# Kernel tuning notes

Hardware: AMD Instinct MI355X
Metric: run time of the kernel (lower is better)

Reference implementation:

```python
import jax, jax.numpy as jnp
import numpy as np

N_LAYERS = 2   # number of S6 blocks
D = 512        # input_dim / d_model
N = 16         # hid_dim (SSM state size)
O = 512        # output_dim
B = 4          # batch
L = 2048       # seq_len
LN_EPS = 1e-5


def setup_inputs() -> dict:
    key = jax.random.key(0)
    ks = jax.random.split(key, 10)
    s = D ** -0.5
    inp = {
        "x": jax.random.normal(ks[0], (B, L, D), jnp.float32),
        # per-layer S6 block params (stacked over layer axis)
        "A_log": jax.random.normal(ks[1], (N_LAYERS, D, N), jnp.float32) * 0.5,
        "W_B": jax.random.normal(ks[2], (N_LAYERS, D, N), jnp.float32) * s,
        "b_B": jnp.zeros((N_LAYERS, N), jnp.float32),
        "W_C": jax.random.normal(ks[3], (N_LAYERS, D, N), jnp.float32) * s,
        "b_C": jnp.zeros((N_LAYERS, N), jnp.float32),
        "W_dt": jax.random.normal(ks[4], (N_LAYERS, D, D), jnp.float32) * s,
        "b_dt": jnp.zeros((N_LAYERS, D), jnp.float32),
        "D_skip": jnp.ones((N_LAYERS, D), jnp.float32),
        # mixing linear + layer norm per layer
        "W_mix": jax.random.normal(ks[5], (N_LAYERS, D, D), jnp.float32) * s,
        "b_mix": jnp.zeros((N_LAYERS, D), jnp.float32),
        "ln_g": jnp.ones((N_LAYERS, D), jnp.float32),
        "ln_b": jnp.zeros((N_LAYERS, D), jnp.float32),
        # final decoder
        "W_dec": jax.random.normal(ks[6], (D, O), jnp.float32) * s,
        "b_dec": jnp.zeros((O,), jnp.float32),
    }
    return inp


def _combine(e1, e2):
    # first-order linear recurrence combine: h <- a*h + u
    a1, u1 = e1
    a2, u2 = e2
    return a1 * a2, a2 * u1 + u2


def reference(x, A_log, W_B, b_B, W_C, b_C, W_dt, b_dt, D_skip,
              W_mix, b_mix, ln_g, ln_b, W_dec, b_dec):
    h_in = x  # [B, L, D]
    for i in range(N_LAYERS):
        # ---- S6 block: input-dependent B, C, dt; diagonal A ----
        A = -jnp.exp(A_log[i])                               # [D, N], negative real
        Bm = h_in @ W_B[i] + b_B[i]                          # [B, L, N]
        Cm = h_in @ W_C[i] + b_C[i]                          # [B, L, N]
        dt = jax.nn.softplus(h_in @ W_dt[i] + b_dt[i])       # [B, L, D]
        # discretize: a_t = exp(dt*A), u_t = dt * B_t * x_t
        a = jnp.exp(dt[..., None] * A)                       # [B, L, D, N]
        u = (dt * h_in)[..., None] * Bm[:, :, None, :]       # [B, L, D, N]
        # parallel scan over sequence axis (Heinsen / Blelloch style)
        _, h = jax.lax.associative_scan(_combine, (a, u), axis=1)
        y = jnp.einsum('bln,bldn->bld', Cm, h) + D_skip[i] * h_in  # [B, L, D]
        # ---- activation (torch.nn.GELU default = exact erf) ----
        y = jax.nn.gelu(y, approximate=False)
        # ---- mixing linear ----
        y = y @ W_mix[i] + b_mix[i]
        # ---- layer norm ----
        mu = jnp.mean(y, axis=-1, keepdims=True)
        var = jnp.var(y, axis=-1, keepdims=True)
        y = (y - mu) / jnp.sqrt(var + LN_EPS) * ln_g[i] + ln_b[i]
        # ---- residual ----
        h_in = h_in + y
    return h_in @ W_dec + b_dec  # [B, L, O]
```

## Files before the change

### kernel.cpp

```cpp
#include <hip/hip_runtime.h>
#include <math.h>

typedef unsigned short u16;
typedef unsigned int u32;
typedef __attribute__((ext_vector_type(8))) short short8;
typedef __attribute__((ext_vector_type(4))) float f32x4;

#define BL 8192
#define DD 512
#define NN 16
#define NCHUNK 64
#define SCH 32
#define ZLD 640

__device__ __forceinline__ u16 f2bf(float f) {
  union { float f; u32 u; } v; v.f = f;
  u32 u = v.u;
  return (u16)((u + 0x7FFFu + ((u >> 16) & 1u)) >> 16);
}

__device__ __forceinline__ void split2(float v, u16* __restrict__ h,
                                       u16* __restrict__ l) {
  union { float f; u32 u; } a; a.f = v;
  u32 hr = (a.u + 0x7FFFu + ((a.u >> 16) & 1u)) & 0xFFFF0000u;
  union { u32 u; float f; } hv; hv.u = hr;
  float r = v - hv.f;
  *h = (u16)(hr >> 16);
  *l = f2bf(r);
}

__device__ __forceinline__ float comb2(u16 h, u16 l) {
  union { u32 u; float f; } a, b;
  a.u = (u32)h << 16; b.u = (u32)l << 16;
  return a.f + b.f;
}

__device__ __forceinline__ float softplus_f(float z) {
  float w = __builtin_amdgcn_exp2f(-1.4426950408889634f * fabsf(z));
  return fmaxf(z, 0.0f) + 0.69314718055994531f * __builtin_amdgcn_logf(1.0f + w);
}

__device__ __forceinline__ float gelu_erf(float y) {
  float ax = fabsf(y) * 0.70710678118654752f;
  float t  = __builtin_amdgcn_rcpf(1.0f + 0.3275911f * ax);
  float e  = __builtin_amdgcn_exp2f(-1.4426950408889634f * ax * ax);
  float p  = ((((1.061405429f * t - 1.453152027f) * t + 1.421413741f) * t
               - 0.284496736f) * t + 0.254829592f) * t;
  float er = copysignf(1.0f - p * e, y);
  return 0.5f * y * (1.0f + er);
}

#define PREP_TOT (4194304 + 655360 + 524288 + 262144 + 1280 + 16384)
__global__ __launch_bounds__(256) void prep_kernel(
    const float* __restrict__ x, const float* __restrict__ A_log,
    const float* __restrict__ W_B, const float* __restrict__ b_B,
    const float* __restrict__ W_C, const float* __restrict__ b_C,
    const float* __restrict__ W_dt, const float* __restrict__ b_dt,
    const float* __restrict__ W_mix, const float* __restrict__ W_dec,
    u16* __restrict__ xh, u16* __restrict__ xl,
    u16* __restrict__ Wch, u16* __restrict__ Wcl,
    u16* __restrict__ Wmh, u16* __restrict__ Wml,
    u16* __restrict__ Wdh, u16* __restrict__ Wdl,
    float* __restrict__ bcat, float* __restrict__ A2)
{
  int i = blockIdx.x * 256 + threadIdx.x;
  if (i >= PREP_TOT) return;
  if (i < 4194304) { split2(x[i], &xh[i], &xl[i]); return; }
  i -= 4194304;
  if (i < 655360) {
    int l = i / 327680, r = i % 327680, n = r >> 9, k = r & 511;
    float v = 0.0f;
    if (n < 16)       v = W_B[l * 8192 + k * 16 + n];
    else if (n < 32)  v = W_C[l * 8192 + k * 16 + (n - 16)];
    else if (n < 544) v = W_dt[l * 262144 + k * 512 + (n - 32)];
    split2(v, &Wch[i], &Wcl[i]);
    return;
  }
  i -= 655360;
  if (i < 524288) {
    int l = i / 262144, r = i % 262144, n = r >> 9, k = r & 511;
    split2(W_mix[l * 262144 + k * 512 + n], &Wmh[i], &Wml[i]);
    return;
  }
  i -= 524288;
  if (i < 262144) {
    int n = i >> 9, k = i & 511;
    split2(W_dec[k * 512 + n], &Wdh[i], &Wdl[i]);
    return;
  }
  i -= 262144;
  if (i < 1280) {
    int l = i / 640, n = i % 640;
    float v = 0.0f;
    if (n < 16)       v = b_B[l * 16 + n];
    else if (n < 32)  v = b_C[l * 16 + (n - 16)];
    else if (n < 544) v = b_dt[l * 512 + (n - 32)];
    bcat[i] = v;
    return;
  }
  i -= 1280;
  A2[i] = -expf(A_log[i]) * 1.4426950408889634f;
}

template <int MODE>
__global__ __launch_bounds__(256) void gemm_bt(
    const u16* __restrict__ Ah, const u16* __restrict__ Al,
    const u16* __restrict__ Bh, const u16* __restrict__ Bl,
    const float* __restrict__ bias, float* __restrict__ Cmat, int ldc,
    int NX)
{
  const int K = 512;
  int bid = blockIdx.x;
  int xcd = bid & 7;
  int rest = bid >> 3;
  int mloc = rest & 7;
  int nb = rest >> 3;
  int m0 = (xcd * 8 + mloc) * 128;
  int n0 = nb * 64;
  __shared__ __align__(16) char smem[36864];
  u16* Ash = (u16*)smem;
  u16* Asl = Ash + 128 * 32;
  u16* Bsh = Asl + 128 * 32;
  u16* Bsl = Bsh + 64 * 32;
  int tid = threadIdx.x;
  int wave = tid >> 6, lane = tid & 63;
  int wm = (wave >> 1) * 64;
  int wn = (wave & 1) * 32;
  int lrow = lane & 15;
  int lk = (lane >> 4) * 8;
  f32x4 acc[4][2] = {};

  int q0 = tid, q1 = tid + 256;
  size_t offA0 = (size_t)(m0 + (q0 >> 2)) * K + (q0 & 3) * 8;
  size_t offA1 = (size_t)(m0 + (q1 >> 2)) * K + (q1 & 3) * 8;
  size_t offB  = (size_t)(n0 + (q0 >> 2)) * K + (q0 & 3) * 8;
  unsigned l0 = (unsigned)(wave * 64) * 8;
  unsigned l1 = (unsigned)(wave * 64 + 256) * 8;

  for (int k0 = 0; k0 < K; k0 += 32) {
    __builtin_amdgcn_global_load_lds(
        (const __attribute__((address_space(1))) void*)(Ah + offA0 + k0),
        (__attribute__((address_space(3))) void*)(&Ash[l0]), 16, 0, 0);
    __builtin_amdgcn_global_load_lds(
        (const __attribute__((address_space(1))) void*)(Ah + offA1 + k0),
        (__attribute__((address_space(3))) void*)(&Ash[l1]), 16, 0, 0);
    __builtin_amdgcn_global_load_lds(
        (const __attribute__((address_space(1))) void*)(Al + offA0 + k0),
        (__attribute__((address_space(3))) void*)(&Asl[l0]), 16, 0, 0);
    __builtin_amdgcn_global_load_lds(
        (const __attribute__((address_space(1))) void*)(Al + offA1 + k0),
        (__attribute__((address_space(3))) void*)(&Asl[l1]), 16, 0, 0);
    __builtin_amdgcn_global_load_lds(
        (const __attribute__((address_space(1))) void*)(Bh + offB + k0),
        (__attribute__((address_space(3))) void*)(&Bsh[l0]), 16, 0, 0);
    __builtin_amdgcn_global_load_lds(
        (const __attribute__((address_space(1))) void*)(Bl + offB + k0),
        (__attribute__((address_space(3))) void*)(&Bsl[l0]), 16, 0, 0);
    __syncthreads();

    short8 afh[4], afl[4], bfh[2], bfl[2];
#pragma unroll
    for (int i = 0; i < 4; ++i) {
      afh[i] = *(const short8*)&Ash[(wm + i * 16 + lrow) * 32 + lk];
      afl[i] = *(const short8*)&Asl[(wm + i * 16 + lrow) * 32 + lk];
    }
#pragma unroll
    for (int t = 0; t < 2; ++t) {
      bfh[t] = *(const short8*)&Bsh[(wn + t * 16 + lrow) * 32 + lk];
      bfl[t] = *(const short8*)&Bsl[(wn + t * 16 + lrow) * 32 + lk];
    }
#pragma unroll
    for (int i = 0; i < 4; ++i)
#pragma unroll
      for (int t = 0; t < 2; ++t) {
        acc[i][t] = __builtin_amdgcn_mfma_f32_16x16x32_bf16(afh[i], bfh[t], acc[i][t], 0, 0, 0);
        acc[i][t] = __builtin_amdgcn_mfma_f32_16x16x32_bf16(afl[i], bfh[t], acc[i][t], 0, 0, 0);
        acc[i][t] = __builtin_amdgcn_mfma_f32_16x16x32_bf16(afh[i], bfl[t], acc[i][t], 0, 0, 0);
      }
    __syncthreads();
  }

  float* ct = (float*)smem + wave * (64 * 36);
  int quad = lane >> 4;
#pragma unroll
  for (int t = 0; t < 2; ++t) {
    int coll = wn + t * 16 + lrow;
    float bv = bias[n0 + coll];
    bool sp = (MODE == 1) && (n0 + coll >= 32);
#pragma unroll
    for (int i = 0; i < 4; ++i) {
#pragma unroll
      for (int r = 0; r < 4; ++r) {
        float v = acc[i][t][r] + bv;
        if (sp) v = softplus_f(v);
        ct[(i * 16 + quad * 4 + r) * 36 + (t * 16 + lrow)] = v;
      }
    }
  }
  __syncthreads();
  int r8 = lane >> 3, c8 = lane & 7;
  int colv = n0 + wn + c8 * 4;
  bool do_store = !(MODE == 1 && colv >= 544);
#pragma unroll
  for (int pass = 0; pass < 8; ++pass) {
    int rowl = pass * 8 + r8;
    float4 v = *(const float4*)&ct[rowl * 36 + c8 * 4];
    if (do_store)
      *(float4*)&Cmat[(size_t)(m0 + wm + rowl) * ldc + colv] = v;
  }
}

template <int PACKED>
__global__ __launch_bounds__(256) void scan_p1(
    const float* __restrict__ Z, const float* __restrict__ Xf,
    const u16* __restrict__ Xh, const u16* __restrict__ Xl,
    const float* __restrict__ A2,
    float* __restrict__ Ach, float* __restrict__ Uch)
{
  int bid = blockIdx.x;
  int dg = bid & 1, c = (bid >> 1) & (NCHUNK - 1), b = bid >> 7;
  int d = dg * 256 + threadIdx.x;
  int row0 = b * 2048 + c * SCH;
  __shared__ float Bsh[SCH * 16];
  for (int i = threadIdx.x; i < SCH * 16; i += 256)
    Bsh[i] = Z[(size_t)(row0 + (i >> 4)) * ZLD + (i & 15)];
  __syncthreads();
  float a2[16];
  const float4* a2v = (const float4*)(A2 + d * 16);
#pragma unroll
  for (int q = 0; q < 4; ++q) {
    float4 f = a2v[q];
    a2[q * 4 + 0] = f.x; a2[q * 4 + 1] = f.y; a2[q * 4 + 2] = f.z; a2[q * 4 + 3] = f.w;
  }
  float ap[16], u[16];
#pragma unroll
  for (int n = 0; n < 16; ++n) { ap[n] = 1.0f; u[n] = 0.0f; }
  for (int t = 0; t < SCH; ++t) {
    size_t row = row0 + t;
    float dtv = Z[row * ZLD + 32 + d];
    float xv = PACKED ? comb2(Xh[row * DD + d], Xl[row * DD + d])
                      : Xf[row * DD + d];
    float dx = dtv * xv;
#pragma unroll
    for (int n = 0; n < 16; ++n) {
      float e = __builtin_amdgcn_exp2f(dtv * a2[n]);
      u[n] = e * u[n] + dx * Bsh[t * 16 + n];
      ap[n] *= e;
    }
  }
  size_t out = ((size_t)(b * NCHUNK + c) * DD + d) * 16;
#pragma unroll
  for (int n = 0; n < 16; ++n) { Ach[out + n] = ap[n]; Uch[out + n] = u[n]; }
}

__global__ __launch_bounds__(256) void scan_p2(
    const float* __restrict__ Ach, float* __restrict__ Uch)
{
  int blk = blockIdx.x;
  int b = blk >> 7;
  int dn = (blk & 127) * 64 + (threadIdx.x & 63);
  int seg = threadIdx.x >> 6;
  size_t base = (size_t)b * NCHUNK * 8192 + dn;
  float a_r[16], u_r[16];
#pragma unroll
  for (int i = 0; i < 16; ++i) {
    size_t idx = base + (size_t)(seg * 16 + i) * 8192;
    a_r[i] = Ach[idx];
    u_r[i] = Uch[idx];
  }
  float Ap = 1.0f, hA = 0.0f;
#pragma unroll
  for (int i = 0; i < 16; ++i) { hA = a_r[i] * hA + u_r[i]; Ap *= a_r[i]; }
  __shared__ float AsegL[4][64], UsegL[4][64];
  AsegL[seg][threadIdx.x & 63] = Ap;
  UsegL[seg][threadIdx.x & 63] = hA;
  __syncthreads();
  float h = 0.0f;
  for (int s = 0; s < seg; ++s)
    h = AsegL[s][threadIdx.x & 63] * h + UsegL[s][threadIdx.x & 63];
#pragma unroll
  for (int i = 0; i < 16; ++i) {
    size_t idx = base + (size_t)(seg * 16 + i) * 8192;
    Uch[idx] = h;
    h = a_r[i] * h + u_r[i];
  }
}

template <int PACKED>
__global__ __launch_bounds__(256) void scan_p3(
    const float* __restrict__ Z, const float* __restrict__ Xf,
    const u16* __restrict__ Xh, const u16* __restrict__ Xl,
    const float* __restrict__ A2, const float* __restrict__ Hinit,
    const float* __restrict__ Dskip,
    u16* __restrict__ Yh, u16* __restrict__ Yl)
{
  int bid = blockIdx.x;
  int dg = bid & 1, c = (bid >> 1) & (NCHUNK - 1), b = bid >> 7;
  int d = dg * 256 + threadIdx.x;
  int row0 = b * 2048 + c * SCH;
  __shared__ float Bsh[SCH * 16];
  __shared__ float Csh[SCH * 16];
  for (int i = threadIdx.x; i < SCH * 16; i += 256) {
    size_t rz = (size_t)(row0 + (i >> 4)) * ZLD;
    Bsh[i] = Z[rz + (i & 15)];
    Csh[i] = Z[rz + 16 + (i & 15)];
  }
  __syncthreads();
  float a2[16];
  const float4* a2v = (const float4*)(A2 + d * 16);
#pragma unroll
  for (int q = 0; q < 4; ++q) {
    float4 f = a2v[q];
    a2[q * 4 + 0] = f.x; a2[q * 4 + 1] = f.y; a2[q * 4 + 2] = f.z; a2[q * 4 + 3] = f.w;
  }
  float h[16];
  size_t hidx = ((size_t)(b * NCHUNK + c) * DD + d) * 16;
#pragma unroll
  for (int n = 0; n < 16; ++n) h[n] = Hinit[hidx + n];
  float dsk = Dskip[d];
  for (int t = 0; t < SCH; ++t) {
    size_t row = row0 + t;
    float dtv = Z[row * ZLD + 32 + d];
    float xv = PACKED ? comb2(Xh[row * DD + d], Xl[row * DD + d])
                      : Xf[row * DD + d];
    float dx = dtv * xv;
    float acc = 0.0f;
#pragma unroll
    for (int n = 0; n < 16; ++n) {
      float e = __builtin_amdgcn_exp2f(dtv * a2[n]);
      h[n] = e * h[n] + dx * Bsh[t * 16 + n];
      acc += Csh[t * 16 + n] * h[n];
    }
    float y = acc + dsk * xv;
    split2(gelu_erf(y), &Yh[row * DD + d], &Yl[row * DD + d]);
  }
}

template <int PACKED>
__global__ __launch_bounds__(256) void ln_residual(
    const float* __restrict__ Y2, const float* Xf,
    const float* __restrict__ gam, const float* __restrict__ bet,
    u16* Hh, u16* Hl)
{
  int wave = threadIdx.x >> 6, lane = threadIdx.x & 63;
  size_t row = (size_t)blockIdx.x * 4 + wave;
  size_t gbase = row * DD + lane * 8;
  const float4* yr = (const float4*)(Y2 + gbase);
  float4 y0 = yr[0], y1 = yr[1];
  float v[8] = {y0.x, y0.y, y0.z, y0.w, y1.x, y1.y, y1.z, y1.w};
  float s = 0.0f, sq = 0.0f;
#pragma unroll
  for (int j = 0; j < 8; ++j) { s += v[j]; sq += v[j] * v[j]; }
#pragma unroll
  for (int off = 32; off; off >>= 1) {
    s += __shfl_xor(s, off, 64);
    sq += __shfl_xor(sq, off, 64);
  }
  float mu = s * (1.0f / 512.0f);
  float var = sq * (1.0f / 512.0f) - mu * mu;
  float rstd = rsqrtf(var + 1e-5f);

  float hin[8];
  if (PACKED) {
    short8 hh = *(const short8*)(Hh + gbase);
    short8 hl = *(const short8*)(Hl + gbase);
#pragma unroll
    for (int j = 0; j < 8; ++j) hin[j] = comb2((u16)hh[j], (u16)hl[j]);
  } else {
    const float4* xr = (const float4*)(Xf + gbase);
    float4 x0 = xr[0], x1 = xr[1];
    hin[0]=x0.x; hin[1]=x0.y; hin[2]=x0.z; hin[3]=x0.w;
    hin[4]=x1.x; hin[5]=x1.y; hin[6]=x1.z; hin[7]=x1.w;
  }
  const float4* g4 = (const float4*)(gam + lane * 8);
  const float4* b4 = (const float4*)(bet + lane * 8);
  float4 g0 = g4[0], g1 = g4[1], bb0 = b4[0], bb1 = b4[1];
  float gv[8] = {g0.x,g0.y,g0.z,g0.w,g1.x,g1.y,g1.z,g1.w};
  float bv[8] = {bb0.x,bb0.y,bb0.z,bb0.w,bb1.x,bb1.y,bb1.z,bb1.w};
  short8 sh, sl;
#pragma unroll
  for (int j = 0; j < 8; ++j) {
    float o = (v[j] - mu) * rstd * gv[j] + bv[j] + hin[j];
    u16 oh, ol;
    split2(o, &oh, &ol);
    sh[j] = (short)oh; sl[j] = (short)ol;
  }
  *(short8*)(Hh + gbase) = sh;
  *(short8*)(Hl + gbase) = sl;
}

extern "C" void kernel_launch(void* const* d_in, const int* in_sizes, int n_in,
                              void* d_out, int out_size, void* d_ws, size_t ws_size,
                              hipStream_t stream) {
  const float* x      = (const float*)d_in[0];
  const float* A_log  = (const float*)d_in[1];
  const float* W_B    = (const float*)d_in[2];
  const float* b_B    = (const float*)d_in[3];
  const float* W_C    = (const float*)d_in[4];
  const float* b_C    = (const float*)d_in[5];
  const float* W_dt   = (const float*)d_in[6];
  const float* b_dt   = (const float*)d_in[7];
  const float* D_skip = (const float*)d_in[8];
  const float* W_mix  = (const float*)d_in[9];
  const float* b_mix  = (const float*)d_in[10];
  const float* ln_g   = (const float*)d_in[11];
  const float* ln_b   = (const float*)d_in[12];
  const float* W_dec  = (const float*)d_in[13];
  const float* b_dec  = (const float*)d_in[14];

  char* ws = (char*)d_ws;
  size_t off = 0;
  u16*   x_hi = (u16*)(ws + off);
  float* Ach  = (float*)(ws + off);
  u16*   y_hi = (u16*)(ws + off); off += 8388608;
  u16*   x_lo = (u16*)(ws + off);
  u16*   y_lo = (u16*)(ws + off); off += 8388608;
  u16*   h_hi = (u16*)(ws + off); off += 8388608;
  u16*   h_lo = (u16*)(ws + off); off += 8388608;
  float* Z    = (float*)(ws + off);
  float* y2   = (float*)(ws + off); off += 20971520;
  float* Uch  = (float*)(ws + off); off += 8388608;
  u16*   Wch  = (u16*)(ws + off);   off += 1310720;
  u16*   Wcl  = (u16*)(ws + off);   off += 1310720;
  u16*   Wmh  = (u16*)(ws + off);   off += 1048576;
  u16*   Wml  = (u16*)(ws + off);   off += 1048576;
  u16*   Wdh  = (u16*)(ws + off);   off += 524288;
  u16*   Wdl  = (u16*)(ws + off);   off += 524288;
  float* bcat = (float*)(ws + off); off += 5120;
  float* A2w  = (float*)(ws + off); off += 65536;

  prep_kernel<<<(PREP_TOT + 255) / 256, 256, 0, stream>>>(
      x, A_log, W_B, b_B, W_C, b_C, W_dt, b_dt, W_mix, W_dec,
      x_hi, x_lo, Wch, Wcl, Wmh, Wml, Wdh, Wdl, bcat, A2w);

  for (int l = 0; l < 2; ++l) {
    const u16* Ahp = (l == 0) ? x_hi : h_hi;
    const u16* Alp = (l == 0) ? x_lo : h_lo;
    gemm_bt<1><<<640, 256, 0, stream>>>(
        Ahp, Alp, Wch + l * 640 * 512, Wcl + l * 640 * 512,
        bcat + l * 640, Z, ZLD, 10);
    if (l == 0) {
      scan_p1<0><<<512, 256, 0, stream>>>(Z, x, nullptr, nullptr,
                                          A2w + l * 8192, Ach, Uch);
      scan_p2<<<512, 256, 0, stream>>>(Ach, Uch);
      scan_p3<0><<<512, 256, 0, stream>>>(Z, x, nullptr, nullptr,
                                          A2w + l * 8192, Uch,
                                          D_skip + l * 512, y_hi, y_lo);
    } else {
      scan_p1<1><<<512, 256, 0, stream>>>(Z, nullptr, h_hi, h_lo,
                                          A2w + l * 8192, Ach, Uch);
      scan_p2<<<512, 256, 0, stream>>>(Ach, Uch);
      scan_p3<1><<<512, 256, 0, stream>>>(Z, nullptr, h_hi, h_lo,
                                          A2w + l * 8192, Uch,
                                          D_skip + l * 512, y_hi, y_lo);
    }
    gemm_bt<0><<<512, 256, 0, stream>>>(
        y_hi, y_lo, Wmh + l * 512 * 512, Wml + l * 512 * 512,
        b_mix + l * 512, y2, DD, 8);
    if (l == 0)
      ln_residual<0><<<2048, 256, 0, stream>>>(y2, x, ln_g + l * 512,
                                               ln_b + l * 512, h_hi, h_lo);
    else
      ln_residual<1><<<2048, 256, 0, stream>>>(y2, nullptr, ln_g + l * 512,
                                               ln_b + l * 512, h_hi, h_lo);
  }
  gemm_bt<0><<<512, 256, 0, stream>>>(
      h_hi, h_lo, Wdh, Wdl, b_dec, (float*)d_out, DD, 8);
}
```

Before: 329.4 us.

## Load GEMM MFMA fragments directly from global memory, bypassing LDS staging

Removes the LDS staging of A/B tiles via global_load_lds and the per-k-step barriers in the split-bf16 GEMM. Each wave now loads its MFMA operand fragments straight from global memory into registers, with the k-loop unrolled by 2. This drops the synchronisation and LDS traffic, but each tile is re-read by several waves through the cache, and the 16-byte row-strided loads are less coalesced. The LDS buffer is kept only for the epilogue transpose, and the unused NX parameter is dropped.

```diff
diff --git a/kernel.cpp b/kernel.cpp
--- a/kernel.cpp
+++ b/kernel.cpp
@@ -106,8 +106,7 @@
 __global__ __launch_bounds__(256) void gemm_bt(
     const u16* __restrict__ Ah, const u16* __restrict__ Al,
     const u16* __restrict__ Bh, const u16* __restrict__ Bl,
-    const float* __restrict__ bias, float* __restrict__ Cmat, int ldc,
-    int NX)
+    const float* __restrict__ bias, float* __restrict__ Cmat, int ldc)
 {
   const int K = 512;
   int bid = blockIdx.x;
@@ -117,57 +116,39 @@
   int nb = rest >> 3;
   int m0 = (xcd * 8 + mloc) * 128;
   int n0 = nb * 64;
-  __shared__ __align__(16) char smem[36864];
-  u16* Ash = (u16*)smem;
-  u16* Asl = Ash + 128 * 32;
-  u16* Bsh = Asl + 128 * 32;
-  u16* Bsl = Bsh + 64 * 32;
+  __shared__ __align__(16) float ctbuf[4 * 64 * 36];
   int tid = threadIdx.x;
   int wave = tid >> 6, lane = tid & 63;
   int wm = (wave >> 1) * 64;
   int wn = (wave & 1) * 32;
   int lrow = lane & 15;
   int lk = (lane >> 4) * 8;
+
+  const u16 *pAh[4], *pAl[4], *pBh[2], *pBl[2];
+#pragma unroll
+  for (int i = 0; i < 4; ++i) {
+    size_t r = (size_t)(m0 + wm + i * 16 + lrow) * K + lk;
+    pAh[i] = Ah + r; pAl[i] = Al + r;
+  }
+#pragma unroll
+  for (int t = 0; t < 2; ++t) {
+    size_t r = (size_t)(n0 + wn + t * 16 + lrow) * K + lk;
+    pBh[t] = Bh + r; pBl[t] = Bl + r;
+  }
   f32x4 acc[4][2] = {};
 
-  int q0 = tid, q1 = tid + 256;
-  size_t offA0 = (size_t)(m0 + (q0 >> 2)) * K + (q0 & 3) * 8;
-  size_t offA1 = (size_t)(m0 + (q1 >> 2)) * K + (q1 & 3) * 8;
-  size_t offB  = (size_t)(n0 + (q0 >> 2)) * K + (q0 & 3) * 8;
-  unsigned l0 = (unsigned)(wave * 64) * 8;
-  unsigned l1 = (unsigned)(wave * 64 + 256) * 8;
-
+#pragma unroll 2
   for (int k0 = 0; k0 < K; k0 += 32) {
-    __builtin_amdgcn_global_load_lds(
-        (const __attribute__((address_space(1))) void*)(Ah + offA0 + k0),
-        (__attribute__((address_space(3))) void*)(&Ash[l0]), 16, 0, 0);
-    __builtin_amdgcn_global_load_lds(
-        (const __attribute__((address_space(1))) void*)(Ah + offA1 + k0),
-        (__attribute__((address_space(3))) void*)(&Ash[l1]), 16, 0, 0);
-    __builtin_amdgcn_global_load_lds(
-        (const __attribute__((address_space(1))) void*)(Al + offA0 + k0),
-        (__attribute__((address_space(3))) void*)(&Asl[l0]), 16, 0, 0);
-    __builtin_amdgcn_global_load_lds(
-        (const __attribute__((address_space(1))) void*)(Al + offA1 + k0),
-        (__attribute__((address_space(3))) void*)(&Asl[l1]), 16, 0, 0);
-    __builtin_amdgcn_global_load_lds(
-        (const __attribute__((address_space(1))) void*)(Bh + offB + k0),
-        (__attribute__((address_space(3))) void*)(&Bsh[l0]), 16, 0, 0);
-    __builtin_amdgcn_global_load_lds(
-        (const __attribute__((address_space(1))) void*)(Bl + offB + k0),
-        (__attribute__((address_space(3))) void*)(&Bsl[l0]), 16, 0, 0);
-    __syncthreads();
-
     short8 afh[4], afl[4], bfh[2], bfl[2];
 #pragma unroll
     for (int i = 0; i < 4; ++i) {
-      afh[i] = *(const short8*)&Ash[(wm + i * 16 + lrow) * 32 + lk];
-      afl[i] = *(const short8*)&Asl[(wm + i * 16 + lrow) * 32 + lk];
+      afh[i] = *(const short8*)(pAh[i] + k0);
+      afl[i] = *(const short8*)(pAl[i] + k0);
     }
 #pragma unroll
     for (int t = 0; t < 2; ++t) {
-      bfh[t] = *(const short8*)&Bsh[(wn + t * 16 + lrow) * 32 + lk];
-      bfl[t] = *(const short8*)&Bsl[(wn + t * 16 + lrow) * 32 + lk];
+      bfh[t] = *(const short8*)(pBh[t] + k0);
+      bfl[t] = *(const short8*)(pBl[t] + k0);
     }
 #pragma unroll
     for (int i = 0; i < 4; ++i)
@@ -177,10 +158,9 @@
         acc[i][t] = __builtin_amdgcn_mfma_f32_16x16x32_bf16(afl[i], bfh[t], acc[i][t], 0, 0, 0);
         acc[i][t] = __builtin_amdgcn_mfma_f32_16x16x32_bf16(afh[i], bfl[t], acc[i][t], 0, 0, 0);
       }
-    __syncthreads();
-  }
-
-  float* ct = (float*)smem + wave * (64 * 36);
+  }
+
+  float* ct = ctbuf + wave * (64 * 36);
   int quad = lane >> 4;
 #pragma unroll
   for (int t = 0; t < 2; ++t) {
@@ -438,7 +418,7 @@
     const u16* Alp = (l == 0) ? x_lo : h_lo;
     gemm_bt<1><<<640, 256, 0, stream>>>(
         Ahp, Alp, Wch + l * 640 * 512, Wcl + l * 640 * 512,
-        bcat + l * 640, Z, ZLD, 10);
+        bcat + l * 640, Z, ZLD);
     if (l == 0) {
       scan_p1<0><<<512, 256, 0, stream>>>(Z, x, nullptr, nullptr,
                                           A2w + l * 8192, Ach, Uch);
@@ -456,7 +436,7 @@
     }
     gemm_bt<0><<<512, 256, 0, stream>>>(
         y_hi, y_lo, Wmh + l * 512 * 512, Wml + l * 512 * 512,
-        b_mix + l * 512, y2, DD, 8);
+        b_mix + l * 512, y2, DD);
     if (l == 0)
       ln_residual<0><<<2048, 256, 0, stream>>>(y2, x, ln_g + l * 512,
                                                ln_b + l * 512, h_hi, h_lo);
@@ -465,5 +445,5 @@
                                                ln_b + l * 512, h_hi, h_lo);
   }
   gemm_bt<0><<<512, 256, 0, stream>>>(
-      h_hi, h_lo, Wdh, Wdl, b_dec, (float*)d_out, DD, 8);
-}
+      h_hi, h_lo, Wdh, Wdl, b_dec, (float*)d_out, DD);
+}
```

Measured after the change: 500.9 us. 52.1% more time.

## Replace split-bf16 three-pass GEMMs with single-pass fp16 MFMA and fp16 activations

Applied to the files above, without the earlier changes.

Drops the hi/lo bf16 splitting scheme, which needed three MFMAs per tile and two buffers per operand. Weights, inputs and the intermediate activations (y, h) are now stored as single fp16 tensors, and each GEMM does one f16 MFMA. This cuts matrix-core work by about two thirds and halves the operand memory traffic in the GEMMs, scan and layernorm kernels. The cost is lower precision, since fp16 has roughly an 11-bit mantissa, and the residual stream is now kept in fp16 between layers. The first GEMM grid also shrinks from 640 to 576 blocks, which drops the padded column tiles beyond 544.

```diff
diff --git a/kernel.cpp b/kernel.cpp
--- a/kernel.cpp
+++ b/kernel.cpp
@@ -4,6 +4,7 @@
 typedef unsigned short u16;
 typedef unsigned int u32;
 typedef __attribute__((ext_vector_type(8))) short short8;
+typedef __attribute__((ext_vector_type(8))) _Float16 half8;
 typedef __attribute__((ext_vector_type(4))) float f32x4;
 
 #define BL 8192
@@ -12,28 +13,6 @@
 #define NCHUNK 64
 #define SCH 32
 #define ZLD 640
-
-__device__ __forceinline__ u16 f2bf(float f) {
-  union { float f; u32 u; } v; v.f = f;
-  u32 u = v.u;
-  return (u16)((u + 0x7FFFu + ((u >> 16) & 1u)) >> 16);
-}
-
-__device__ __forceinline__ void split2(float v, u16* __restrict__ h,
-                                       u16* __restrict__ l) {
-  union { float f; u32 u; } a; a.f = v;
-  u32 hr = (a.u + 0x7FFFu + ((a.u >> 16) & 1u)) & 0xFFFF0000u;
-  union { u32 u; float f; } hv; hv.u = hr;
-  float r = v - hv.f;
-  *h = (u16)(hr >> 16);
-  *l = f2bf(r);
-}
-
-__device__ __forceinline__ float comb2(u16 h, u16 l) {
-  union { u32 u; float f; } a, b;
-  a.u = (u32)h << 16; b.u = (u32)l << 16;
-  return a.f + b.f;
-}
 
 __device__ __forceinline__ float softplus_f(float z) {
   float w = __builtin_amdgcn_exp2f(-1.4426950408889634f * fabsf(z));
@@ -57,15 +36,13 @@
     const float* __restrict__ W_C, const float* __restrict__ b_C,
     const float* __restrict__ W_dt, const float* __restrict__ b_dt,
     const float* __restrict__ W_mix, const float* __restrict__ W_dec,
-    u16* __restrict__ xh, u16* __restrict__ xl,
-    u16* __restrict__ Wch, u16* __restrict__ Wcl,
-    u16* __restrict__ Wmh, u16* __restrict__ Wml,
-    u16* __restrict__ Wdh, u16* __restrict__ Wdl,
+    _Float16* __restrict__ x16, _Float16* __restrict__ Wc16,
+    _Float16* __restrict__ Wm16, _Float16* __restrict__ Wd16,
     float* __restrict__ bcat, float* __restrict__ A2)
 {
   int i = blockIdx.x * 256 + threadIdx.x;
   if (i >= PREP_TOT) return;
-  if (i < 4194304) { split2(x[i], &xh[i], &xl[i]); return; }
+  if (i < 4194304) { x16[i] = (_Float16)x[i]; return; }
   i -= 4194304;
   if (i < 655360) {
     int l = i / 327680, r = i % 327680, n = r >> 9, k = r & 511;
@@ -73,19 +50,19 @@
     if (n < 16)       v = W_B[l * 8192 + k * 16 + n];
     else if (n < 32)  v = W_C[l * 8192 + k * 16 + (n - 16)];
     else if (n < 544) v = W_dt[l * 262144 + k * 512 + (n - 32)];
-    split2(v, &Wch[i], &Wcl[i]);
+    Wc16[i] = (_Float16)v;
     return;
   }
   i -= 655360;
   if (i < 524288) {
     int l = i / 262144, r = i % 262144, n = r >> 9, k = r & 511;
-    split2(W_mix[l * 262144 + k * 512 + n], &Wmh[i], &Wml[i]);
+    Wm16[i] = (_Float16)W_mix[l * 262144 + k * 512 + n];
     return;
   }
   i -= 524288;
   if (i < 262144) {
     int n = i >> 9, k = i & 511;
-    split2(W_dec[k * 512 + n], &Wdh[i], &Wdl[i]);
+    Wd16[i] = (_Float16)W_dec[k * 512 + n];
     return;
   }
   i -= 262144;
@@ -103,11 +80,9 @@
 }
 
 template <int MODE>
-__global__ __launch_bounds__(256) void gemm_bt(
-    const u16* __restrict__ Ah, const u16* __restrict__ Al,
-    const u16* __restrict__ Bh, const u16* __restrict__ Bl,
-    const float* __restrict__ bias, float* __restrict__ Cmat, int ldc,
-    int NX)
+__global__ __launch_bounds__(256) void gemm_f16(
+    const _Float16* __restrict__ A, const _Float16* __restrict__ Bt,
+    const float* __restrict__ bias, float* __restrict__ Cmat, int ldc)
 {
   const int K = 512;
   int bid = blockIdx.x;
@@ -118,10 +93,8 @@
   int m0 = (xcd * 8 + mloc) * 128;
   int n0 = nb * 64;
   __shared__ __align__(16) char smem[36864];
-  u16* Ash = (u16*)smem;
-  u16* Asl = Ash + 128 * 32;
-  u16* Bsh = Asl + 128 * 32;
-  u16* Bsl = Bsh + 64 * 32;
+  _Float16* As = (_Float16*)smem;
+  _Float16* Bs = As + 128 * 32;
   int tid = threadIdx.x;
   int wave = tid >> 6, lane = tid & 63;
   int wm = (wave >> 1) * 64;
@@ -139,44 +112,28 @@
 
   for (int k0 = 0; k0 < K; k0 += 32) {
     __builtin_amdgcn_global_load_lds(
-        (const __attribute__((address_space(1))) void*)(Ah + offA0 + k0),
-        (__attribute__((address_space(3))) void*)(&Ash[l0]), 16, 0, 0);
+        (const __attribute__((address_space(1))) void*)(A + offA0 + k0),
+        (__attribute__((address_space(3))) void*)(&As[l0]), 16, 0, 0);
     __builtin_amdgcn_global_load_lds(
-        (const __attribute__((address_space(1))) void*)(Ah + offA1 + k0),
-        (__attribute__((address_space(3))) void*)(&Ash[l1]), 16, 0, 0);
+        (const __attribute__((address_space(1))) void*)(A + offA1 + k0),
+        (__attribute__((address_space(3))) void*)(&As[l1]), 16, 0, 0);
     __builtin_amdgcn_global_load_lds(
-        (const __attribute__((address_space(1))) void*)(Al + offA0 + k0),
-        (__attribute__((address_space(3))) void*)(&Asl[l0]), 16, 0, 0);
-    __builtin_amdgcn_global_load_lds(
-        (const __attribute__((address_space(1))) void*)(Al + offA1 + k0),
-        (__attribute__((address_space(3))) void*)(&Asl[l1]), 16, 0, 0);
-    __builtin_amdgcn_global_load_lds(
-        (const __attribute__((address_space(1))) void*)(Bh + offB + k0),
-        (__attribute__((address_space(3))) void*)(&Bsh[l0]), 16, 0, 0);
-    __builtin_amdgcn_global_load_lds(
-        (const __attribute__((address_space(1))) void*)(Bl + offB + k0),
-        (__attribute__((address_space(3))) void*)(&Bsl[l0]), 16, 0, 0);
+        (const __attribute__((address_space(1))) void*)(Bt + offB + k0),
+        (__attribute__((address_space(3))) void*)(&Bs[l0]), 16, 0, 0);
     __syncthreads();
 
-    short8 afh[4], afl[4], bfh[2], bfl[2];
-#pragma unroll
-    for (int i = 0; i < 4; ++i) {
-      afh[i] = *(const short8*)&Ash[(wm + i * 16 + lrow) * 32 + lk];
-      afl[i] = *(const short8*)&Asl[(wm + i * 16 + lrow) * 32 + lk];
-    }
-#pragma unroll
-    for (int t = 0; t < 2; ++t) {
-      bfh[t] = *(const short8*)&Bsh[(wn + t * 16 + lrow) * 32 + lk];
-      bfl[t] = *(const short8*)&Bsl[(wn + t * 16 + lrow) * 32 + lk];
-    }
+    half8 af[4], bf[2];
 #pragma unroll
     for (int i = 0; i < 4; ++i)
-#pragma unroll
-      for (int t = 0; t < 2; ++t) {
-        acc[i][t] = __builtin_amdgcn_mfma_f32_16x16x32_bf16(afh[i], bfh[t], acc[i][t], 0, 0, 0);
-        acc[i][t] = __builtin_amdgcn_mfma_f32_16x16x32_bf16(afl[i], bfh[t], acc[i][t], 0, 0, 0);
-        acc[i][t] = __builtin_amdgcn_mfma_f32_16x16x32_bf16(afh[i], bfl[t], acc[i][t], 0, 0, 0);
-      }
+      af[i] = *(const half8*)&As[(wm + i * 16 + lrow) * 32 + lk];
+#pragma unroll
+    for (int t = 0; t < 2; ++t)
+      bf[t] = *(const half8*)&Bs[(wn + t * 16 + lrow) * 32 + lk];
+#pragma unroll
+    for (int i = 0; i < 4; ++i)
+#pragma unroll
+      for (int t = 0; t < 2; ++t)
+        acc[i][t] = __builtin_amdgcn_mfma_f32_16x16x32_f16(af[i], bf[t], acc[i][t], 0, 0, 0);
     __syncthreads();
   }
 
@@ -213,8 +170,7 @@
 template <int PACKED>
 __global__ __launch_bounds__(256) void scan_p1(
     const float* __restrict__ Z, const float* __restrict__ Xf,
-    const u16* __restrict__ Xh, const u16* __restrict__ Xl,
-    const float* __restrict__ A2,
+    const _Float16* __restrict__ Xh, const float* __restrict__ A2,
     float* __restrict__ Ach, float* __restrict__ Uch)
 {
   int bid = blockIdx.x;
@@ -238,8 +194,7 @@
   for (int t = 0; t < SCH; ++t) {
     size_t row = row0 + t;
     float dtv = Z[row * ZLD + 32 + d];
-    float xv = PACKED ? comb2(Xh[row * DD + d], Xl[row * DD + d])
-                      : Xf[row * DD + d];
+    float xv = PACKED ? (float)Xh[row * DD + d] : Xf[row * DD + d];
     float dx = dtv * xv;
 #pragma unroll
     for (int n = 0; n < 16; ++n) {
@@ -289,10 +244,9 @@
 template <int PACKED>
 __global__ __launch_bounds__(256) void scan_p3(
     const float* __restrict__ Z, const float* __restrict__ Xf,
-    const u16* __restrict__ Xh, const u16* __restrict__ Xl,
-    const float* __restrict__ A2, const float* __restrict__ Hinit,
-    const float* __restrict__ Dskip,
-    u16* __restrict__ Yh, u16* __restrict__ Yl)
+    const _Float16* __restrict__ Xh, const float* __restrict__ A2,
+    const float* __restrict__ Hinit, const float* __restrict__ Dskip,
+    _Float16* __restrict__ Yout)
 {
   int bid = blockIdx.x;
   int dg = bid & 1, c = (bid >> 1) & (NCHUNK - 1), b = bid >> 7;
@@ -321,8 +275,7 @@
   for (int t = 0; t < SCH; ++t) {
     size_t row = row0 + t;
     float dtv = Z[row * ZLD + 32 + d];
-    float xv = PACKED ? comb2(Xh[row * DD + d], Xl[row * DD + d])
-                      : Xf[row * DD + d];
+    float xv = PACKED ? (float)Xh[row * DD + d] : Xf[row * DD + d];
     float dx = dtv * xv;
     float acc = 0.0f;
 #pragma unroll
@@ -332,7 +285,7 @@
       acc += Csh[t * 16 + n] * h[n];
     }
     float y = acc + dsk * xv;
-    split2(gelu_erf(y), &Yh[row * DD + d], &Yl[row * DD + d]);
+    Yout[row * DD + d] = (_Float16)gelu_erf(y);
   }
 }
 
@@ -340,7 +293,7 @@
 __global__ __launch_bounds__(256) void ln_residual(
     const float* __restrict__ Y2, const float* Xf,
     const float* __restrict__ gam, const float* __restrict__ bet,
-    u16* Hh, u16* Hl)
+    _Float16* Hh)
 {
   int wave = threadIdx.x >> 6, lane = threadIdx.x & 63;
   size_t row = (size_t)blockIdx.x * 4 + wave;
@@ -362,10 +315,9 @@
 
   float hin[8];
   if (PACKED) {
-    short8 hh = *(const short8*)(Hh + gbase);
-    short8 hl = *(const short8*)(Hl + gbase);
-#pragma unroll
-    for (int j = 0; j < 8; ++j) hin[j] = comb2((u16)hh[j], (u16)hl[j]);
+    half8 hh = *(const half8*)(Hh + gbase);
+#pragma unroll
+    for (int j = 0; j < 8; ++j) hin[j] = (float)hh[j];
   } else {
     const float4* xr = (const float4*)(Xf + gbase);
     float4 x0 = xr[0], x1 = xr[1];
@@ -377,16 +329,13 @@
   float4 g0 = g4[0], g1 = g4[1], bb0 = b4[0], bb1 = b4[1];
   float gv[8] = {g0.x,g0.y,g0.z,g0.w,g1.x,g1.y,g1.z,g1.w};
   float bv[8] = {bb0.x,bb0.y,bb0.z,bb0.w,bb1.x,bb1.y,bb1.z,bb1.w};
-  short8 sh, sl;
+  half8 sh;
 #pragma unroll
   for (int j = 0; j < 8; ++j) {
     float o = (v[j] - mu) * rstd * gv[j] + bv[j] + hin[j];
-    u16 oh, ol;
-    split2(o, &oh, &ol);
-    sh[j] = (short)oh; sl[j] = (short)ol;
-  }
-  *(short8*)(Hh + gbase) = sh;
-  *(short8*)(Hl + gbase) = sl;
+    sh[j] = (_Float16)o;
+  }
+  *(half8*)(Hh + gbase) = sh;
 }
 
 extern "C" void kernel_launch(void* const* d_in, const int* in_sizes, int n_in,
@@ -410,60 +359,49 @@
 
   char* ws = (char*)d_ws;
   size_t off = 0;
-  u16*   x_hi = (u16*)(ws + off);
-  float* Ach  = (float*)(ws + off);
-  u16*   y_hi = (u16*)(ws + off); off += 8388608;
-  u16*   x_lo = (u16*)(ws + off);
-  u16*   y_lo = (u16*)(ws + off); off += 8388608;
-  u16*   h_hi = (u16*)(ws + off); off += 8388608;
-  u16*   h_lo = (u16*)(ws + off); off += 8388608;
+  _Float16* x16 = (_Float16*)(ws + off);
+  float*    Ach = (float*)(ws + off);     off += 8388608;
+  _Float16* y16 = (_Float16*)(ws + off);  off += 8388608;
+  _Float16* h16 = (_Float16*)(ws + off);  off += 8388608;
   float* Z    = (float*)(ws + off);
   float* y2   = (float*)(ws + off); off += 20971520;
   float* Uch  = (float*)(ws + off); off += 8388608;
-  u16*   Wch  = (u16*)(ws + off);   off += 1310720;
-  u16*   Wcl  = (u16*)(ws + off);   off += 1310720;
-  u16*   Wmh  = (u16*)(ws + off);   off += 1048576;
-  u16*   Wml  = (u16*)(ws + off);   off += 1048576;
-  u16*   Wdh  = (u16*)(ws + off);   off += 524288;
-  u16*   Wdl  = (u16*)(ws + off);   off += 524288;
+  _Float16* Wc16 = (_Float16*)(ws + off); off += 1310720;
+  _Float16* Wm16 = (_Float16*)(ws + off); off += 1048576;
+  _Float16* Wd16 = (_Float16*)(ws + off); off += 524288;
   float* bcat = (float*)(ws + off); off += 5120;
   float* A2w  = (float*)(ws + off); off += 65536;
 
   prep_kernel<<<(PREP_TOT + 255) / 256, 256, 0, stream>>>(
       x, A_log, W_B, b_B, W_C, b_C, W_dt, b_dt, W_mix, W_dec,
-      x_hi, x_lo, Wch, Wcl, Wmh, Wml, Wdh, Wdl, bcat, A2w);
+      x16, Wc16, Wm16, Wd16, bcat, A2w);
 
   for (int l = 0; l < 2; ++l) {
-    const u16* Ahp = (l == 0) ? x_hi : h_hi;
-    const u16* Alp = (l == 0) ? x_lo : h_lo;
-    gemm_bt<1><<<640, 256, 0, stream>>>(
-        Ahp, Alp, Wch + l * 640 * 512, Wcl + l * 640 * 512,
-        bcat + l * 640, Z, ZLD, 10);
+    const _Float16* Ain = (l == 0) ? x16 : h16;
+    gemm_f16<1><<<576, 256, 0, stream>>>(
+        Ain, Wc16 + l * 640 * 512, bcat + l * 640, Z, ZLD);
     if (l == 0) {
-      scan_p1<0><<<512, 256, 0, stream>>>(Z, x, nullptr, nullptr,
+      scan_p1<0><<<512, 256, 0, stream>>>(Z, x, nullptr,
                                           A2w + l * 8192, Ach, Uch);
       scan_p2<<<512, 256, 0, stream>>>(Ach, Uch);
-      scan_p3<0><<<512, 256, 0, stream>>>(Z, x, nullptr, nullptr,
-                                          A2w + l * 8192, Uch,
-                                          D_skip + l * 512, y_hi, y_lo);
+      scan_p3<0><<<512, 256, 0, stream>>>(Z, x, nullptr, A2w + l * 8192,
+                                          Uch, D_skip + l * 512, y16);
     } else {
-      scan_p1<1><<<512, 256, 0, stream>>>(Z, nullptr, h_hi, h_lo,
+      scan_p1<1><<<512, 256, 0, stream>>>(Z, nullptr, h16,
                                           A2w + l * 8192, Ach, Uch);
       scan_p2<<<512, 256, 0, stream>>>(Ach, Uch);
-      scan_p3<1><<<512, 256, 0, stream>>>(Z, nullptr, h_hi, h_lo,
-                                          A2w + l * 8192, Uch,
-                                          D_skip + l * 512, y_hi, y_lo);
+      scan_p3<1><<<512, 256, 0, stream>>>(Z, nullptr, h16, A2w + l * 8192,
+                                          Uch, D_skip + l * 512, y16);
     }
-    gemm_bt<0><<<512, 256, 0, stream>>>(
-        y_hi, y_lo, Wmh + l * 512 * 512, Wml + l * 512 * 512,
-        b_mix + l * 512, y2, DD, 8);
+    gemm_f16<0><<<512, 256, 0, stream>>>(
+        y16, Wm16 + l * 512 * 512, b_mix + l * 512, y2, DD);
     if (l == 0)
       ln_residual<0><<<2048, 256, 0, stream>>>(y2, x, ln_g + l * 512,
-                                               ln_b + l * 512, h_hi, h_lo);
+                                               ln_b + l * 512, h16);
     else
       ln_residual<1><<<2048, 256, 0, stream>>>(y2, nullptr, ln_g + l * 512,
-                                               ln_b + l * 512, h_hi, h_lo);
-  }
-  gemm_bt<0><<<512, 256, 0, stream>>>(
-      h_hi, h_lo, Wdh, Wdl, b_dec, (float*)d_out, DD, 8);
-}
+                                               ln_b + l * 512, h16);
+  }
+  gemm_f16<0><<<512, 256, 0, stream>>>(
+      h16, Wd16, b_dec, (float*)d_out, DD);
+}
```

Result: faster. 291.3 us (-11.6%).
